# Performance work log

Hardware: AMD Instinct MI355X
Metric: run time of the kernel (lower is better)

The kernel has to match this reference:

```python
import jax, jax.numpy as jnp
import numpy as np

B, N, DIM_IN, DIM_OUT, CHEB_K, EMBED_DIM = 64, 2048, 64, 64, 3, 10


def setup_inputs() -> dict:
    key = jax.random.key(0)
    k1, k2, k3, k4 = jax.random.split(key, 4)
    x = jax.random.normal(k1, (B, N, DIM_IN), dtype=jnp.float32)
    node_embeddings = jax.random.normal(k2, (N, EMBED_DIM), dtype=jnp.float32)
    # xavier-normal-like init for the pools
    w_std = (2.0 / (EMBED_DIM * CHEB_K * DIM_IN + DIM_OUT)) ** 0.5
    b_std = (2.0 / (EMBED_DIM + DIM_OUT)) ** 0.5
    weights_pool = jax.random.normal(k3, (EMBED_DIM, CHEB_K, DIM_IN, DIM_OUT), dtype=jnp.float32) * w_std
    bias_pool = jax.random.normal(k4, (EMBED_DIM, DIM_OUT), dtype=jnp.float32) * b_std
    return {"x": x, "node_embeddings": node_embeddings,
            "weights_pool": weights_pool, "bias_pool": bias_pool,
            "cheb_k": CHEB_K}


def reference(x, node_embeddings, weights_pool, bias_pool, cheb_k):
    n = node_embeddings.shape[0]
    # adaptive adjacency: softmax(relu(E E^T)) over neighbors
    supports = jax.nn.softmax(jax.nn.relu(node_embeddings @ node_embeddings.T), axis=1)
    # Chebyshev polynomial supports: T0 = I, T1 = A, Tk = 2 A T_{k-1} - T_{k-2}
    support_set = [jnp.eye(n, dtype=supports.dtype), supports]
    for _ in range(2, cheb_k):
        support_set.append(2.0 * supports @ support_set[-1] - support_set[-2])
    supports_k = jnp.stack(support_set, axis=0)  # [K, N, N]
    # per-node weights and bias synthesized from node embeddings
    weights = jnp.einsum('nd,dkio->nkio', node_embeddings, weights_pool)  # [N, K, I, O]
    bias = node_embeddings @ bias_pool                                    # [N, O]
    # graph convolution
    x_g = jnp.einsum('knm,bmc->bnkc', supports_k, x)                      # [B, N, K, I]
    out = jnp.einsum('bnki,nkio->bno', x_g, weights) + bias               # [B, N, O]
    return out
```

## Files before the change

kernel.cpp:

```cpp
#include <hip/hip_runtime.h>

#define NN 2048
#define BB 64
#define CC 64
#define ED 10
#define KK 3
#define JJ (BB * CC)

typedef unsigned short ushort_t;
typedef __attribute__((ext_vector_type(8))) short short8;
typedef __attribute__((ext_vector_type(4))) float f32x4;

typedef const __attribute__((address_space(1))) unsigned* gptr_t;
typedef __attribute__((address_space(3))) unsigned* lptr_t;

static __device__ __forceinline__ ushort_t f2bf(float f) {
    union { float f; unsigned u; } x{f};
    unsigned r = x.u + 0x7FFF + ((x.u >> 16) & 1);
    return (ushort_t)(r >> 16);
}
static __device__ __forceinline__ float bf2f(ushort_t h) {
    union { unsigned u; float f; } x;
    x.u = ((unsigned)h) << 16;
    return x.f;
}

__global__ __launch_bounds__(256) void prep_kernel(const float* __restrict__ E,
                                                   const float* __restrict__ x,
                                                   const float* __restrict__ Wp,
                                                   ushort_t* __restrict__ Ab,
                                                   ushort_t* __restrict__ xT,
                                                   ushort_t* __restrict__ xN,
                                                   ushort_t* __restrict__ WpT) {
    const int bid = blockIdx.x;
    const int tid = threadIdx.x;

    __shared__ float tb[64][68];
    __shared__ float red[8];

    if (bid < NN) {
        const int n = bid;
        float en[ED];
#pragma unroll
        for (int d = 0; d < ED; ++d) en[d] = E[n * ED + d];

        float sv[NN / 256];
        float lmax = 0.0f;
#pragma unroll
        for (int j = 0; j < NN / 256; ++j) {
            const int m = tid + j * 256;
            const float* Em = E + m * ED;
            float dot = 0.0f;
#pragma unroll
            for (int d = 0; d < ED; ++d) dot += en[d] * Em[d];
            float s = fmaxf(dot, 0.0f);
            sv[j] = s;
            lmax = fmaxf(lmax, s);
        }
#pragma unroll
        for (int off = 32; off > 0; off >>= 1) lmax = fmaxf(lmax, __shfl_down(lmax, off, 64));
        if ((tid & 63) == 0) red[tid >> 6] = lmax;
        __syncthreads();
        const float bmax = fmaxf(fmaxf(red[0], red[1]), fmaxf(red[2], red[3]));

        float lsum = 0.0f;
#pragma unroll
        for (int j = 0; j < NN / 256; ++j) {
            sv[j] = __expf(sv[j] - bmax);
            lsum += sv[j];
        }
#pragma unroll
        for (int off = 32; off > 0; off >>= 1) lsum += __shfl_down(lsum, off, 64);
        if ((tid & 63) == 0) red[4 + (tid >> 6)] = lsum;
        __syncthreads();
        const float inv = 1.0f / (red[4] + red[5] + red[6] + red[7]);

#pragma unroll
        for (int j = 0; j < NN / 256; ++j) {
            Ab[(size_t)n * NN + tid + j * 256] = f2bf(sv[j] * inv);
        }
    } else if (bid < 2 * NN) {
        const int t = bid - NN;
        const int n0 = (t & 31) * 64;
        const int b = t >> 5;

#pragma unroll
        for (int l = 0; l < 4; ++l) {
            const int idx = tid + l * 256;
            const int nn = idx >> 4;
            const int c4 = (idx & 15) << 2;
            const float4 v = *(const float4*)(x + ((size_t)b * NN + n0 + nn) * CC + c4);
            tb[c4 + 0][nn] = v.x;
            tb[c4 + 1][nn] = v.y;
            tb[c4 + 2][nn] = v.z;
            tb[c4 + 3][nn] = v.w;
        }
        __syncthreads();

#pragma unroll
        for (int l = 0; l < 2; ++l) {
            const int idx = tid + l * 256;
            const int c = idx >> 3;
            const int ch = (idx & 7) << 3;
            ushort_t pack[8];
#pragma unroll
            for (int e = 0; e < 8; ++e) pack[e] = f2bf(tb[c][ch + e]);
            *(float4*)(xT + (size_t)(b * 64 + c) * NN + n0 + ch) = *(float4*)pack;
        }
#pragma unroll
        for (int l = 0; l < 2; ++l) {
            const int idx = tid + l * 256;
            const int nn = idx >> 3;
            const int cg = (idx & 7) << 3;
            ushort_t pack[8];
#pragma unroll
            for (int e = 0; e < 8; ++e) pack[e] = f2bf(tb[cg + e][nn]);
            *(float4*)(xN + (size_t)(n0 + nn) * JJ + b * 64 + cg) = *(float4*)pack;
        }
    } else {
        const int dk = bid - 2 * NN;
        const float* src = Wp + (size_t)dk * CC * CC;

#pragma unroll
        for (int l = 0; l < 4; ++l) {
            const int idx = tid + l * 256;
            const int i = idx >> 4;
            const int o4 = (idx & 15) << 2;
            const float4 v = *(const float4*)(src + i * CC + o4);
            tb[o4 + 0][i] = v.x;
            tb[o4 + 1][i] = v.y;
            tb[o4 + 2][i] = v.z;
            tb[o4 + 3][i] = v.w;
        }
        __syncthreads();

#pragma unroll
        for (int l = 0; l < 2; ++l) {
            const int idx = tid + l * 256;
            const int o = idx >> 3;
            const int ic = (idx & 7) << 3;
            ushort_t pack[8];
#pragma unroll
            for (int e = 0; e < 8; ++e) pack[e] = f2bf(tb[o][ic + e]);
            *(float4*)(WpT + (size_t)dk * CC * CC + o * CC + ic) = *(float4*)pack;
        }
    }
}

template <int MODE>
__global__ __launch_bounds__(256) void gemm_nt(const ushort_t* __restrict__ A,
                                               const ushort_t* __restrict__ Bt,
                                               const ushort_t* __restrict__ Zn,
                                               ushort_t* __restrict__ Ct,
                                               ushort_t* __restrict__ Cn) {
    const int j0 = blockIdx.x * 128;
    const int m0 = blockIdx.y * 128;
    const int tid = threadIdx.x;
    const int lane = tid & 63;
    const int l16 = lane & 15;
    const int quad = lane >> 4;
    const int w = tid >> 6;
    const int wm = (w >> 1) * 64;
    const int wj = (w & 1) * 64;
    const int lr = lane >> 3;
    const int lc = lane & 7;
    const int swz = lc ^ lr;

    __shared__ ushort_t As[2][128 * 64];
    __shared__ ushort_t Bs[2][128 * 64];

    f32x4 acc[4][4];
#pragma unroll
    for (int mi = 0; mi < 4; ++mi)
#pragma unroll
        for (int ji = 0; ji < 4; ++ji) acc[mi][ji] = (f32x4){0.f, 0.f, 0.f, 0.f};

#pragma unroll
    for (int inst = 0; inst < 4; ++inst) {
        const int rbase = w * 32 + inst * 8;
        const int row = rbase + lr;
        __builtin_amdgcn_global_load_lds(
            (gptr_t)(A + (size_t)(m0 + row) * NN + swz * 8),
            (lptr_t)&As[0][rbase * 64], 16, 0, 0);
        __builtin_amdgcn_global_load_lds(
            (gptr_t)(Bt + (size_t)(j0 + row) * NN + swz * 8),
            (lptr_t)&Bs[0][rbase * 64], 16, 0, 0);
    }

    for (int it = 0; it < NN / 64; ++it) {
        const int cur = it & 1;
        __syncthreads();

        if (it + 1 < NN / 64) {
            const int k0 = (it + 1) * 64;
#pragma unroll
            for (int inst = 0; inst < 4; ++inst) {
                const int rbase = w * 32 + inst * 8;
                const int row = rbase + lr;
                __builtin_amdgcn_global_load_lds(
                    (gptr_t)(A + (size_t)(m0 + row) * NN + k0 + swz * 8),
                    (lptr_t)&As[1 - cur][rbase * 64], 16, 0, 0);
                __builtin_amdgcn_global_load_lds(
                    (gptr_t)(Bt + (size_t)(j0 + row) * NN + k0 + swz * 8),
                    (lptr_t)&Bs[1 - cur][rbase * 64], 16, 0, 0);
            }
        }

#pragma unroll
        for (int ks = 0; ks < 64; ks += 32) {
            const int qb = (ks >> 3) + quad;
            short8 av[4], bv[4];
#pragma unroll
            for (int mi = 0; mi < 4; ++mi) {
                const int rA = wm + mi * 16 + l16;
                av[mi] = *(const short8*)&As[cur][rA * 64 + ((qb ^ (rA & 7)) << 3)];
            }
#pragma unroll
            for (int ji = 0; ji < 4; ++ji) {
                const int rB = wj + ji * 16 + l16;
                bv[ji] = *(const short8*)&Bs[cur][rB * 64 + ((qb ^ (rB & 7)) << 3)];
            }
#pragma unroll
            for (int mi = 0; mi < 4; ++mi)
#pragma unroll
                for (int ji = 0; ji < 4; ++ji)
                    acc[mi][ji] = __builtin_amdgcn_mfma_f32_16x16x32_bf16(
                        av[mi], bv[ji], acc[mi][ji], 0, 0, 0);
        }
    }

#pragma unroll
    for (int mi = 0; mi < 4; ++mi) {
#pragma unroll
        for (int ji = 0; ji < 4; ++ji) {
            const int j = j0 + wj + ji * 16 + l16;
            const int mb = m0 + wm + mi * 16 + quad * 4;
            if (MODE == 0) {
                ushort_t o[4];
#pragma unroll
                for (int r = 0; r < 4; ++r) o[r] = f2bf(acc[mi][ji][r]);
                *(unsigned long long*)(Ct + (size_t)j * NN + mb) = *(unsigned long long*)o;
#pragma unroll
                for (int r = 0; r < 4; ++r) Cn[(size_t)(mb + r) * JJ + j] = o[r];
            } else {
#pragma unroll
                for (int r = 0; r < 4; ++r) {
                    const float z = bf2f(Zn[(size_t)(mb + r) * JJ + j]);
                    Cn[(size_t)(mb + r) * JJ + j] = f2bf(2.0f * acc[mi][ji][r] - z);
                }
            }
        }
    }
}

#define XLD 200
__global__ __launch_bounds__(256) void out_kernel(const float* __restrict__ E,
                                                  const ushort_t* __restrict__ WpT,
                                                  const float* __restrict__ bp,
                                                  const ushort_t* __restrict__ xN,
                                                  const ushort_t* __restrict__ y1N,
                                                  const ushort_t* __restrict__ y2N,
                                                  float* __restrict__ out) {
    const int n = blockIdx.x;
    const int tid = threadIdx.x;

    __shared__ ushort_t xg[BB * XLD];
    __shared__ ushort_t Wt[CC * XLD];
    __shared__ float en_s[ED];
    __shared__ float bias_s[CC];

    if (tid < ED) en_s[tid] = E[n * ED + tid];
    __syncthreads();

    float en[ED];
#pragma unroll
    for (int d = 0; d < ED; ++d) en[d] = en_s[d];

    if (tid < CC) {
        float bsum = 0.0f;
#pragma unroll
        for (int d = 0; d < ED; ++d) bsum += en[d] * bp[d * CC + tid];
        bias_s[tid] = bsum;
    }

#pragma unroll
    for (int k = 0; k < KK; ++k) {
        const ushort_t* src = (k == 0) ? xN : (k == 1) ? y1N : y2N;
        const float4* srow = (const float4*)(src + (size_t)n * JJ);
        for (int idx = tid; idx < JJ / 8; idx += 256) {
            *(float4*)&xg[(idx >> 3) * XLD + k * 64 + ((idx & 7) << 3)] = srow[idx];
        }
    }

    for (int t = tid; t < CC * 24; t += 256) {
        const int o = t / 24;
        const int kc = t % 24;
        const int k = kc >> 3;
        const int ic = (kc & 7) << 3;
        float s[8];
#pragma unroll
        for (int e = 0; e < 8; ++e) s[e] = 0.0f;
#pragma unroll
        for (int d = 0; d < ED; ++d) {
            const float4 wv4 = *(const float4*)(WpT + ((size_t)(d * KK + k) * CC + o) * CC + ic);
            const ushort_t* wp = (const ushort_t*)&wv4;
#pragma unroll
            for (int e = 0; e < 8; ++e) s[e] += en[d] * bf2f(wp[e]);
        }
        ushort_t pack[8];
#pragma unroll
        for (int e = 0; e < 8; ++e) pack[e] = f2bf(s[e]);
        *(float4*)&Wt[o * XLD + k * 64 + ic] = *(float4*)pack;
    }
    __syncthreads();

    const int lane = tid & 63;
    const int l16 = lane & 15;
    const int quad = lane >> 4;
    const int bm = (tid >> 6) * 16;

    f32x4 acc[4];
#pragma unroll
    for (int ji = 0; ji < 4; ++ji) acc[ji] = (f32x4){0.f, 0.f, 0.f, 0.f};

#pragma unroll
    for (int kc = 0; kc < 6; ++kc) {
        const short8 av = *(const short8*)&xg[(bm + l16) * XLD + kc * 32 + quad * 8];
#pragma unroll
        for (int ji = 0; ji < 4; ++ji) {
            const short8 bv = *(const short8*)&Wt[(ji * 16 + l16) * XLD + kc * 32 + quad * 8];
            acc[ji] = __builtin_amdgcn_mfma_f32_16x16x32_bf16(av, bv, acc[ji], 0, 0, 0);
        }
    }

#pragma unroll
    for (int ji = 0; ji < 4; ++ji) {
        const int o = ji * 16 + l16;
        const float bo = bias_s[o];
#pragma unroll
        for (int r = 0; r < 4; ++r) {
            const int b = bm + quad * 4 + r;
            out[((size_t)b * NN + n) * CC + o] = acc[ji][r] + bo;
        }
    }
}
#undef XLD

extern "C" void kernel_launch(void* const* d_in, const int* in_sizes, int n_in,
                              void* d_out, int out_size, void* d_ws, size_t ws_size,
                              hipStream_t stream) {
    const float* x  = (const float*)d_in[0];
    const float* E  = (const float*)d_in[1];
    const float* Wp = (const float*)d_in[2];
    const float* bp = (const float*)d_in[3];

    ushort_t* Ab  = (ushort_t*)d_ws;
    ushort_t* xT  = Ab + (size_t)NN * NN;
    ushort_t* xN  = xT + (size_t)JJ * NN;
    ushort_t* y1T = xN + (size_t)NN * JJ;
    ushort_t* y1N = y1T + (size_t)JJ * NN;
    ushort_t* y2N = y1N + (size_t)NN * JJ;
    ushort_t* WpT = y2N + (size_t)NN * JJ;
    float* out = (float*)d_out;

    prep_kernel<<<2 * NN + ED * KK, 256, 0, stream>>>(E, x, Wp, Ab, xT, xN, WpT);
    gemm_nt<0><<<dim3(JJ / 128, NN / 128), 256, 0, stream>>>(Ab, xT, nullptr, y1T, y1N);
    gemm_nt<1><<<dim3(JJ / 128, NN / 128), 256, 0, stream>>>(Ab, y1T, xN, nullptr, y2N);
    out_kernel<<<NN, 256, 0, stream>>>(E, WpT, bp, xN, y1N, y2N, out);
}
```

Before: 218.1 us.

## Use 8 waves in GEMM and batch four nodes per out_kernel block

The two large GEMMs now launch 512 threads (8 waves) per 128x128 tile, each wave owning 32x64 outputs instead of 64x64, which halves per-wave accumulators and load work and raises the number of waves available to hide latency. The output kernel processes four nodes per block, one per wave, looping over the Chebyshev order k and rebuilding the per-node weights for all four nodes from a single load of the weight pool. This reuses the weight-pool reads across nodes and gives each wave a full 64x64 MFMA tile. In exchange it adds extra barriers per k step and more LDS per block, which can lower occupancy.

```diff
diff --git a/kernel.cpp b/kernel.cpp
--- a/kernel.cpp
+++ b/kernel.cpp
@@ -148,7 +148,7 @@
 }
 
 template <int MODE>
-__global__ __launch_bounds__(256) void gemm_nt(const ushort_t* __restrict__ A,
+__global__ __launch_bounds__(512) void gemm_nt(const ushort_t* __restrict__ A,
                                                const ushort_t* __restrict__ Bt,
                                                const ushort_t* __restrict__ Zn,
                                                ushort_t* __restrict__ Ct,
@@ -160,7 +160,7 @@
     const int l16 = lane & 15;
     const int quad = lane >> 4;
     const int w = tid >> 6;
-    const int wm = (w >> 1) * 64;
+    const int wm = (w >> 1) * 32;
     const int wj = (w & 1) * 64;
     const int lr = lane >> 3;
     const int lc = lane & 7;
@@ -169,15 +169,15 @@
     __shared__ ushort_t As[2][128 * 64];
     __shared__ ushort_t Bs[2][128 * 64];
 
-    f32x4 acc[4][4];
-#pragma unroll
-    for (int mi = 0; mi < 4; ++mi)
+    f32x4 acc[2][4];
+#pragma unroll
+    for (int mi = 0; mi < 2; ++mi)
 #pragma unroll
         for (int ji = 0; ji < 4; ++ji) acc[mi][ji] = (f32x4){0.f, 0.f, 0.f, 0.f};
 
 #pragma unroll
-    for (int inst = 0; inst < 4; ++inst) {
-        const int rbase = w * 32 + inst * 8;
+    for (int inst = 0; inst < 2; ++inst) {
+        const int rbase = w * 16 + inst * 8;
         const int row = rbase + lr;
         __builtin_amdgcn_global_load_lds(
             (gptr_t)(A + (size_t)(m0 + row) * NN + swz * 8),
@@ -194,8 +194,8 @@
         if (it + 1 < NN / 64) {
             const int k0 = (it + 1) * 64;
 #pragma unroll
-            for (int inst = 0; inst < 4; ++inst) {
-                const int rbase = w * 32 + inst * 8;
+            for (int inst = 0; inst < 2; ++inst) {
+                const int rbase = w * 16 + inst * 8;
                 const int row = rbase + lr;
                 __builtin_amdgcn_global_load_lds(
                     (gptr_t)(A + (size_t)(m0 + row) * NN + k0 + swz * 8),
@@ -209,9 +209,9 @@
 #pragma unroll
         for (int ks = 0; ks < 64; ks += 32) {
             const int qb = (ks >> 3) + quad;
-            short8 av[4], bv[4];
-#pragma unroll
-            for (int mi = 0; mi < 4; ++mi) {
+            short8 av[2], bv[4];
+#pragma unroll
+            for (int mi = 0; mi < 2; ++mi) {
                 const int rA = wm + mi * 16 + l16;
                 av[mi] = *(const short8*)&As[cur][rA * 64 + ((qb ^ (rA & 7)) << 3)];
             }
@@ -221,7 +221,7 @@
                 bv[ji] = *(const short8*)&Bs[cur][rB * 64 + ((qb ^ (rB & 7)) << 3)];
             }
 #pragma unroll
-            for (int mi = 0; mi < 4; ++mi)
+            for (int mi = 0; mi < 2; ++mi)
 #pragma unroll
                 for (int ji = 0; ji < 4; ++ji)
                     acc[mi][ji] = __builtin_amdgcn_mfma_f32_16x16x32_bf16(
@@ -230,7 +230,7 @@
     }
 
 #pragma unroll
-    for (int mi = 0; mi < 4; ++mi) {
+    for (int mi = 0; mi < 2; ++mi) {
 #pragma unroll
         for (int ji = 0; ji < 4; ++ji) {
             const int j = j0 + wj + ji * 16 + l16;
@@ -253,7 +253,8 @@
     }
 }
 
-#define XLD 200
+#define ONPB 4
+#define OLD 72
 __global__ __launch_bounds__(256) void out_kernel(const float* __restrict__ E,
                                                   const ushort_t* __restrict__ WpT,
                                                   const float* __restrict__ bp,
@@ -261,90 +262,114 @@
                                                   const ushort_t* __restrict__ y1N,
                                                   const ushort_t* __restrict__ y2N,
                                                   float* __restrict__ out) {
-    const int n = blockIdx.x;
+    const int n0 = blockIdx.x * ONPB;
     const int tid = threadIdx.x;
 
-    __shared__ ushort_t xg[BB * XLD];
-    __shared__ ushort_t Wt[CC * XLD];
-    __shared__ float en_s[ED];
-    __shared__ float bias_s[CC];
-
-    if (tid < ED) en_s[tid] = E[n * ED + tid];
+    __shared__ ushort_t xg[ONPB][CC * OLD];
+    __shared__ ushort_t Wt[ONPB][CC * OLD];
+    __shared__ float es[ONPB][ED];
+    __shared__ float bias_s[ONPB][CC];
+
+    if (tid < ONPB * ED) es[tid / ED][tid % ED] = E[(size_t)(n0 + tid / ED) * ED + tid % ED];
     __syncthreads();
 
-    float en[ED];
-#pragma unroll
-    for (int d = 0; d < ED; ++d) en[d] = en_s[d];
-
-    if (tid < CC) {
-        float bsum = 0.0f;
-#pragma unroll
-        for (int d = 0; d < ED; ++d) bsum += en[d] * bp[d * CC + tid];
-        bias_s[tid] = bsum;
-    }
-
-#pragma unroll
-    for (int k = 0; k < KK; ++k) {
-        const ushort_t* src = (k == 0) ? xN : (k == 1) ? y1N : y2N;
-        const float4* srow = (const float4*)(src + (size_t)n * JJ);
-        for (int idx = tid; idx < JJ / 8; idx += 256) {
-            *(float4*)&xg[(idx >> 3) * XLD + k * 64 + ((idx & 7) << 3)] = srow[idx];
-        }
-    }
-
-    for (int t = tid; t < CC * 24; t += 256) {
-        const int o = t / 24;
-        const int kc = t % 24;
-        const int k = kc >> 3;
-        const int ic = (kc & 7) << 3;
-        float s[8];
-#pragma unroll
-        for (int e = 0; e < 8; ++e) s[e] = 0.0f;
-#pragma unroll
-        for (int d = 0; d < ED; ++d) {
-            const float4 wv4 = *(const float4*)(WpT + ((size_t)(d * KK + k) * CC + o) * CC + ic);
-            const ushort_t* wp = (const ushort_t*)&wv4;
-#pragma unroll
-            for (int e = 0; e < 8; ++e) s[e] += en[d] * bf2f(wp[e]);
-        }
-        ushort_t pack[8];
-#pragma unroll
-        for (int e = 0; e < 8; ++e) pack[e] = f2bf(s[e]);
-        *(float4*)&Wt[o * XLD + k * 64 + ic] = *(float4*)pack;
-    }
-    __syncthreads();
+    {
+        const int nl = tid >> 6;
+        const int o = tid & 63;
+        float b = 0.0f;
+#pragma unroll
+        for (int d = 0; d < ED; ++d) b += es[nl][d] * bp[d * CC + o];
+        bias_s[nl][o] = b;
+    }
 
     const int lane = tid & 63;
     const int l16 = lane & 15;
     const int quad = lane >> 4;
-    const int bm = (tid >> 6) * 16;
-
-    f32x4 acc[4];
-#pragma unroll
-    for (int ji = 0; ji < 4; ++ji) acc[ji] = (f32x4){0.f, 0.f, 0.f, 0.f};
-
-#pragma unroll
-    for (int kc = 0; kc < 6; ++kc) {
-        const short8 av = *(const short8*)&xg[(bm + l16) * XLD + kc * 32 + quad * 8];
+    const int w = tid >> 6;
+
+    f32x4 acc[4][4];
+#pragma unroll
+    for (int mi = 0; mi < 4; ++mi)
+#pragma unroll
+        for (int ji = 0; ji < 4; ++ji) acc[mi][ji] = (f32x4){0.f, 0.f, 0.f, 0.f};
+
+    for (int k = 0; k < KK; ++k) {
+        const ushort_t* src = (k == 0) ? xN : (k == 1) ? y1N : y2N;
+        __syncthreads();
+
+        for (int t = tid; t < ONPB * 512; t += 256) {
+            const int nl = t >> 9;
+            const int c = t & 511;
+            *(float4*)&xg[nl][(c >> 3) * OLD + ((c & 7) << 3)] =
+                *(const float4*)(src + (size_t)(n0 + nl) * JJ + c * 8);
+        }
+        for (int t = tid; t < 512; t += 256) {
+            const int o = t >> 3;
+            const int ic = (t & 7) << 3;
+            float a4[ONPB][8];
+#pragma unroll
+            for (int nl = 0; nl < ONPB; ++nl)
+#pragma unroll
+                for (int e = 0; e < 8; ++e) a4[nl][e] = 0.0f;
+#pragma unroll
+            for (int d = 0; d < ED; ++d) {
+                const float4 p = *(const float4*)(WpT + ((size_t)(d * KK + k) * CC + o) * CC + ic);
+                const ushort_t* pp = (const ushort_t*)&p;
+                float u[8];
+#pragma unroll
+                for (int e = 0; e < 8; ++e) u[e] = bf2f(pp[e]);
+#pragma unroll
+                for (int nl = 0; nl < ONPB; ++nl) {
+                    const float ed = es[nl][d];
+#pragma unroll
+                    for (int e = 0; e < 8; ++e) a4[nl][e] += ed * u[e];
+                }
+            }
+#pragma unroll
+            for (int nl = 0; nl < ONPB; ++nl) {
+                ushort_t pk[8];
+#pragma unroll
+                for (int e = 0; e < 8; ++e) pk[e] = f2bf(a4[nl][e]);
+                *(float4*)&Wt[nl][o * OLD + ic] = *(float4*)pk;
+            }
+        }
+        __syncthreads();
+
+#pragma unroll
+        for (int ks = 0; ks < 64; ks += 32) {
+            short8 av[4], bv[4];
+#pragma unroll
+            for (int mi = 0; mi < 4; ++mi)
+                av[mi] = *(const short8*)&xg[w][(mi * 16 + l16) * OLD + ks + quad * 8];
+#pragma unroll
+            for (int ji = 0; ji < 4; ++ji)
+                bv[ji] = *(const short8*)&Wt[w][(ji * 16 + l16) * OLD + ks + quad * 8];
+#pragma unroll
+            for (int mi = 0; mi < 4; ++mi)
+#pragma unroll
+                for (int ji = 0; ji < 4; ++ji)
+                    acc[mi][ji] = __builtin_amdgcn_mfma_f32_16x16x32_bf16(
+                        av[mi], bv[ji], acc[mi][ji], 0, 0, 0);
+        }
+    }
+
+    const int n = n0 + w;
+#pragma unroll
+    for (int mi = 0; mi < 4; ++mi) {
 #pragma unroll
         for (int ji = 0; ji < 4; ++ji) {
-            const short8 bv = *(const short8*)&Wt[(ji * 16 + l16) * XLD + kc * 32 + quad * 8];
-            acc[ji] = __builtin_amdgcn_mfma_f32_16x16x32_bf16(av, bv, acc[ji], 0, 0, 0);
-        }
-    }
-
-#pragma unroll
-    for (int ji = 0; ji < 4; ++ji) {
-        const int o = ji * 16 + l16;
-        const float bo = bias_s[o];
-#pragma unroll
-        for (int r = 0; r < 4; ++r) {
-            const int b = bm + quad * 4 + r;
-            out[((size_t)b * NN + n) * CC + o] = acc[ji][r] + bo;
-        }
-    }
-}
-#undef XLD
+            const int o = ji * 16 + l16;
+            const float bo = bias_s[w][o];
+#pragma unroll
+            for (int r = 0; r < 4; ++r) {
+                const int b = mi * 16 + quad * 4 + r;
+                out[((size_t)b * NN + n) * CC + o] = acc[mi][ji][r] + bo;
+            }
+        }
+    }
+}
+#undef OLD
+#undef ONPB
 
 extern "C" void kernel_launch(void* const* d_in, const int* in_sizes, int n_in,
                               void* d_out, int out_size, void* d_ws, size_t ws_size,
@@ -364,7 +389,7 @@
     float* out = (float*)d_out;
 
     prep_kernel<<<2 * NN + ED * KK, 256, 0, stream>>>(E, x, Wp, Ab, xT, xN, WpT);
-    gemm_nt<0><<<dim3(JJ / 128, NN / 128), 256, 0, stream>>>(Ab, xT, nullptr, y1T, y1N);
-    gemm_nt<1><<<dim3(JJ / 128, NN / 128), 256, 0, stream>>>(Ab, y1T, xN, nullptr, y2N);
-    out_kernel<<<NN, 256, 0, stream>>>(E, WpT, bp, xN, y1N, y2N, out);
-}
+    gemm_nt<0><<<dim3(JJ / 128, NN / 128), 512, 0, stream>>>(Ab, xT, nullptr, y1T, y1N);
+    gemm_nt<1><<<dim3(JJ / 128, NN / 128), 512, 0, stream>>>(Ab, y1T, xN, nullptr, y2N);
+    out_kernel<<<NN / 4, 256, 0, stream>>>(E, WpT, bp, xN, y1N, y2N, out);
+}
```

Measured after the change: 232.5 us. +6.6%, slower.

## Use 8 waves in GEMM tiles and load out_kernel activations directly into registers

Applied to the files above, without the earlier changes.

The GEMM kernel now runs 512 threads (8 waves) per 128x128 tile, so each wave computes a 32x64 subtile and issues half as many async loads. The aim is to hide more latency and improve MFMA issue overlap, at the cost of fewer accumulators per wave and less reuse of LDS fragments. out_kernel no longer stages activations in LDS. Each wave loads its A fragments straight from global memory into registers, which cuts LDS traffic and footprint and adds an occupancy hint of 4.

```diff
diff --git a/kernel.cpp b/kernel.cpp
--- a/kernel.cpp
+++ b/kernel.cpp
@@ -148,7 +148,7 @@
 }
 
 template <int MODE>
-__global__ __launch_bounds__(256) void gemm_nt(const ushort_t* __restrict__ A,
+__global__ __launch_bounds__(512) void gemm_nt(const ushort_t* __restrict__ A,
                                                const ushort_t* __restrict__ Bt,
                                                const ushort_t* __restrict__ Zn,
                                                ushort_t* __restrict__ Ct,
@@ -160,7 +160,7 @@
     const int l16 = lane & 15;
     const int quad = lane >> 4;
     const int w = tid >> 6;
-    const int wm = (w >> 1) * 64;
+    const int wm = (w >> 1) * 32;
     const int wj = (w & 1) * 64;
     const int lr = lane >> 3;
     const int lc = lane & 7;
@@ -169,15 +169,15 @@
     __shared__ ushort_t As[2][128 * 64];
     __shared__ ushort_t Bs[2][128 * 64];
 
-    f32x4 acc[4][4];
-#pragma unroll
-    for (int mi = 0; mi < 4; ++mi)
+    f32x4 acc[2][4];
+#pragma unroll
+    for (int mi = 0; mi < 2; ++mi)
 #pragma unroll
         for (int ji = 0; ji < 4; ++ji) acc[mi][ji] = (f32x4){0.f, 0.f, 0.f, 0.f};
 
 #pragma unroll
-    for (int inst = 0; inst < 4; ++inst) {
-        const int rbase = w * 32 + inst * 8;
+    for (int inst = 0; inst < 2; ++inst) {
+        const int rbase = w * 16 + inst * 8;
         const int row = rbase + lr;
         __builtin_amdgcn_global_load_lds(
             (gptr_t)(A + (size_t)(m0 + row) * NN + swz * 8),
@@ -194,8 +194,8 @@
         if (it + 1 < NN / 64) {
             const int k0 = (it + 1) * 64;
 #pragma unroll
-            for (int inst = 0; inst < 4; ++inst) {
-                const int rbase = w * 32 + inst * 8;
+            for (int inst = 0; inst < 2; ++inst) {
+                const int rbase = w * 16 + inst * 8;
                 const int row = rbase + lr;
                 __builtin_amdgcn_global_load_lds(
                     (gptr_t)(A + (size_t)(m0 + row) * NN + k0 + swz * 8),
@@ -209,9 +209,9 @@
 #pragma unroll
         for (int ks = 0; ks < 64; ks += 32) {
             const int qb = (ks >> 3) + quad;
-            short8 av[4], bv[4];
-#pragma unroll
-            for (int mi = 0; mi < 4; ++mi) {
+            short8 av[2], bv[4];
+#pragma unroll
+            for (int mi = 0; mi < 2; ++mi) {
                 const int rA = wm + mi * 16 + l16;
                 av[mi] = *(const short8*)&As[cur][rA * 64 + ((qb ^ (rA & 7)) << 3)];
             }
@@ -221,7 +221,7 @@
                 bv[ji] = *(const short8*)&Bs[cur][rB * 64 + ((qb ^ (rB & 7)) << 3)];
             }
 #pragma unroll
-            for (int mi = 0; mi < 4; ++mi)
+            for (int mi = 0; mi < 2; ++mi)
 #pragma unroll
                 for (int ji = 0; ji < 4; ++ji)
                     acc[mi][ji] = __builtin_amdgcn_mfma_f32_16x16x32_bf16(
@@ -230,7 +230,7 @@
     }
 
 #pragma unroll
-    for (int mi = 0; mi < 4; ++mi) {
+    for (int mi = 0; mi < 2; ++mi) {
 #pragma unroll
         for (int ji = 0; ji < 4; ++ji) {
             const int j = j0 + wj + ji * 16 + l16;
@@ -253,28 +253,44 @@
     }
 }
 
-#define XLD 200
-__global__ __launch_bounds__(256) void out_kernel(const float* __restrict__ E,
-                                                  const ushort_t* __restrict__ WpT,
-                                                  const float* __restrict__ bp,
-                                                  const ushort_t* __restrict__ xN,
-                                                  const ushort_t* __restrict__ y1N,
-                                                  const ushort_t* __restrict__ y2N,
-                                                  float* __restrict__ out) {
+#define OLD 200
+__global__ __launch_bounds__(256, 4) void out_kernel(const float* __restrict__ E,
+                                                     const ushort_t* __restrict__ WpT,
+                                                     const float* __restrict__ bp,
+                                                     const ushort_t* __restrict__ xN,
+                                                     const ushort_t* __restrict__ y1N,
+                                                     const ushort_t* __restrict__ y2N,
+                                                     float* __restrict__ out) {
     const int n = blockIdx.x;
     const int tid = threadIdx.x;
-
-    __shared__ ushort_t xg[BB * XLD];
-    __shared__ ushort_t Wt[CC * XLD];
-    __shared__ float en_s[ED];
+    const int lane = tid & 63;
+    const int l16 = lane & 15;
+    const int quad = lane >> 4;
+    const int w = tid >> 6;
+
+    __shared__ ushort_t Wt[CC * OLD];
+    __shared__ float es[ED];
     __shared__ float bias_s[CC];
 
-    if (tid < ED) en_s[tid] = E[n * ED + tid];
+    if (tid < ED) es[tid] = E[n * ED + tid];
+
+    short8 av[6];
+    {
+        const ushort_t* s0 = xN + (size_t)n * JJ + (w * 16 + l16) * 64;
+        const ushort_t* s1 = y1N + (size_t)n * JJ + (w * 16 + l16) * 64;
+        const ushort_t* s2 = y2N + (size_t)n * JJ + (w * 16 + l16) * 64;
+        av[0] = *(const short8*)(s0 + quad * 8);
+        av[1] = *(const short8*)(s0 + 32 + quad * 8);
+        av[2] = *(const short8*)(s1 + quad * 8);
+        av[3] = *(const short8*)(s1 + 32 + quad * 8);
+        av[4] = *(const short8*)(s2 + quad * 8);
+        av[5] = *(const short8*)(s2 + 32 + quad * 8);
+    }
     __syncthreads();
 
     float en[ED];
 #pragma unroll
-    for (int d = 0; d < ED; ++d) en[d] = en_s[d];
+    for (int d = 0; d < ED; ++d) en[d] = es[d];
 
     if (tid < CC) {
         float bsum = 0.0f;
@@ -283,20 +299,11 @@
         bias_s[tid] = bsum;
     }
 
-#pragma unroll
-    for (int k = 0; k < KK; ++k) {
-        const ushort_t* src = (k == 0) ? xN : (k == 1) ? y1N : y2N;
-        const float4* srow = (const float4*)(src + (size_t)n * JJ);
-        for (int idx = tid; idx < JJ / 8; idx += 256) {
-            *(float4*)&xg[(idx >> 3) * XLD + k * 64 + ((idx & 7) << 3)] = srow[idx];
-        }
-    }
-
     for (int t = tid; t < CC * 24; t += 256) {
         const int o = t / 24;
-        const int kc = t % 24;
-        const int k = kc >> 3;
-        const int ic = (kc & 7) << 3;
+        const int kc8 = t % 24;
+        const int k = kc8 >> 3;
+        const int ic = (kc8 & 7) << 3;
         float s[8];
 #pragma unroll
         for (int e = 0; e < 8; ++e) s[e] = 0.0f;
@@ -310,26 +317,20 @@
         ushort_t pack[8];
 #pragma unroll
         for (int e = 0; e < 8; ++e) pack[e] = f2bf(s[e]);
-        *(float4*)&Wt[o * XLD + k * 64 + ic] = *(float4*)pack;
+        *(float4*)&Wt[o * OLD + kc8 * 8] = *(float4*)pack;
     }
     __syncthreads();
 
-    const int lane = tid & 63;
-    const int l16 = lane & 15;
-    const int quad = lane >> 4;
-    const int bm = (tid >> 6) * 16;
-
     f32x4 acc[4];
 #pragma unroll
     for (int ji = 0; ji < 4; ++ji) acc[ji] = (f32x4){0.f, 0.f, 0.f, 0.f};
 
 #pragma unroll
     for (int kc = 0; kc < 6; ++kc) {
-        const short8 av = *(const short8*)&xg[(bm + l16) * XLD + kc * 32 + quad * 8];
 #pragma unroll
         for (int ji = 0; ji < 4; ++ji) {
-            const short8 bv = *(const short8*)&Wt[(ji * 16 + l16) * XLD + kc * 32 + quad * 8];
-            acc[ji] = __builtin_amdgcn_mfma_f32_16x16x32_bf16(av, bv, acc[ji], 0, 0, 0);
+            const short8 bv = *(const short8*)&Wt[(ji * 16 + l16) * OLD + kc * 32 + quad * 8];
+            acc[ji] = __builtin_amdgcn_mfma_f32_16x16x32_bf16(av[kc], bv, acc[ji], 0, 0, 0);
         }
     }
 
@@ -339,12 +340,12 @@
         const float bo = bias_s[o];
 #pragma unroll
         for (int r = 0; r < 4; ++r) {
-            const int b = bm + quad * 4 + r;
+            const int b = w * 16 + quad * 4 + r;
             out[((size_t)b * NN + n) * CC + o] = acc[ji][r] + bo;
         }
     }
 }
-#undef XLD
+#undef OLD
 
 extern "C" void kernel_launch(void* const* d_in, const int* in_sizes, int n_in,
                               void* d_out, int out_size, void* d_ws, size_t ws_size,
@@ -364,7 +365,7 @@
     float* out = (float*)d_out;
 
     prep_kernel<<<2 * NN + ED * KK, 256, 0, stream>>>(E, x, Wp, Ab, xT, xN, WpT);
-    gemm_nt<0><<<dim3(JJ / 128, NN / 128), 256, 0, stream>>>(Ab, xT, nullptr, y1T, y1N);
-    gemm_nt<1><<<dim3(JJ / 128, NN / 128), 256, 0, stream>>>(Ab, y1T, xN, nullptr, y2N);
+    gemm_nt<0><<<dim3(JJ / 128, NN / 128), 512, 0, stream>>>(Ab, xT, nullptr, y1T, y1N);
+    gemm_nt<1><<<dim3(JJ / 128, NN / 128), 512, 0, stream>>>(Ab, y1T, xN, nullptr, y2N);
     out_kernel<<<NN, 256, 0, stream>>>(E, WpT, bp, xN, y1N, y2N, out);
 }
```

Result: slower. 224.0 us (+2.7%).
